# Performance work log

Hardware: AMD Instinct MI355X
Metric: run time of the kernel (lower is better)

## Reference

```python
import jax, jax.numpy as jnp
from jax import lax
import numpy as np

DILATIONS = [2 ** i for i in range(9)] * 2  # 18 layers
WIDTH = 16
K = 3


def softsign(v):
    return v / (1.0 + jnp.abs(v))


def setup_inputs() -> dict:
    key = jax.random.key(0)
    ks = jax.random.split(key, 9)
    B, T = 4, 65536
    n = len(DILATIONS)
    inp = {
        "x": jax.random.normal(ks[0], (B, 1, T), dtype=jnp.float32),
        "start_w": jax.random.normal(ks[1], (WIDTH, 1), dtype=jnp.float32) * 0.5,
        "conv_w": jax.random.normal(ks[2], (n, WIDTH, WIDTH, K), dtype=jnp.float32) * 0.1,
        "conv_b": jax.random.normal(ks[3], (n, WIDTH), dtype=jnp.float32) * 0.1,
        "gate_w": jax.random.normal(ks[4], (n, WIDTH, WIDTH, K), dtype=jnp.float32) * 0.1,
        "gate_b": jax.random.normal(ks[5], (n, WIDTH), dtype=jnp.float32) * 0.1,
        "res_w": jax.random.normal(ks[6], (n - 1, WIDTH, WIDTH), dtype=jnp.float32) * 0.1,
        "res_b": jax.random.normal(ks[7], (n - 1, WIDTH), dtype=jnp.float32) * 0.1,
        "mixer_w": jax.random.normal(ks[8], (1, WIDTH * n), dtype=jnp.float32) * 0.1,
    }
    return inp


def _dilated_causal_conv(h, w, b, d):
    # h: [B,C,T], w: [O,I,K], causal left pad d*(K-1)
    y = lax.conv_general_dilated(
        h, w, window_strides=(1,), padding=[(d * (K - 1), 0)],
        rhs_dilation=(d,), dimension_numbers=("NCH", "OIH", "NCH"))
    return y + b[None, :, None]


def reference(x, start_w, conv_w, conv_b, gate_w, gate_b, res_w, res_b, mixer_w):
    # start 1x1 conv (no bias): [B,1,T] -> [B,W,T]
    h = jnp.einsum("oi,bit->bot", start_w, x)
    outs = []
    n = len(DILATIONS)
    for li, d in enumerate(DILATIONS):
        f = softsign(_dilated_causal_conv(h, conv_w[li], conv_b[li], d))
        g = softsign(_dilated_causal_conv(h, gate_w[li], gate_b[li], d))
        z = f * g
        outs.append(z)
        if li < n - 1:
            h = h + jnp.einsum("oi,bit->bot", res_w[li], z) + res_b[li][None, :, None]
    skip = jnp.concatenate(outs, axis=1)  # [B, W*n, T]
    return jnp.einsum("oc,bct->bot", mixer_w, skip)  # [B,1,T]
```

## Files before the change

kernel.cpp:

```cpp
#include <hip/hip_runtime.h>
#include <hip/hip_bf16.h>
#include <math.h>


typedef __attribute__((ext_vector_type(8))) short short8;
typedef __attribute__((ext_vector_type(4))) unsigned short ushort4v;
typedef __attribute__((ext_vector_type(16))) float f32x16;
typedef unsigned long long u64;

constexpr int TL = 65536;
constexpr int NTOT = 262144;
constexpr int NBLK = 1024;
constexpr size_t PLANE = 4194304;

__device__ __forceinline__ unsigned short f2bf(float v) {
    __hip_bfloat16 b = __float2bfloat16(v);
    unsigned short u; __builtin_memcpy(&u, &b, 2); return u;
}
__device__ __forceinline__ float bf2f(unsigned int u) {
    unsigned int x = (u & 0xffffu) << 16;
    float f; __builtin_memcpy(&f, &x, 4); return f;
}
__device__ __forceinline__ float softsign_f(float v) {
    return v * __builtin_amdgcn_rcpf(1.0f + fabsf(v));
}
__device__ __forceinline__ void spin_on(const unsigned int* f) {
    while (__hip_atomic_load((unsigned int*)f, __ATOMIC_RELAXED,
                             __HIP_MEMORY_SCOPE_AGENT) == 0u) {
        __builtin_amdgcn_s_sleep(8);
    }
}
__device__ __forceinline__ u64 cohload(const unsigned short* p) {
    return __hip_atomic_load((u64*)p, __ATOMIC_RELAXED, __HIP_MEMORY_SCOPE_AGENT);
}
__device__ __forceinline__ void cohstore(unsigned short* p, u64 v) {
    __hip_atomic_store((u64*)p, v, __ATOMIC_RELAXED, __HIP_MEMORY_SCOPE_AGENT);
}

__global__ __launch_bounds__(256) void pack_kernel(
    const float* __restrict__ start_w,
    const float* __restrict__ conv_w,
    const float* __restrict__ gate_w,
    const float* __restrict__ res_w,
    const float* __restrict__ conv_b,
    const float* __restrict__ gate_b,
    unsigned short* __restrict__ bfrag,
    float* __restrict__ fgbias,
    float* __restrict__ rwp,
    float* __restrict__ e0f, float* __restrict__ e0g)
{
    int idx = blockIdx.x * 256 + threadIdx.x;
    if (idx < 55296) {
        int li = idx / 3072, r = idx % 3072;
        int tap = r / 1024, r2 = r % 1024;
        int p = r2 / 512, r3 = r2 % 512;
        int lane = r3 / 8, j = r3 % 8;
        int n = lane & 31, kh = lane >> 5;
        int i_ch = kh * 8 + j, o = n & 15;
        const float* src = (n < 16) ? conv_w : gate_w;
        float w = src[((li * 16 + o) * 16 + i_ch) * 3 + tap];
        unsigned short hi = f2bf(w);
        bfrag[idx] = (p == 0) ? hi : f2bf(w - bf2f(hi));
    } else if (idx < 55296 + 576) {
        int u = idx - 55296; int li = u / 32, n = u % 32;
        fgbias[u] = (n < 16) ? conv_b[li * 16 + n] : gate_b[li * 16 + n - 16];
    } else if (idx < 55296 + 576 + 4352) {
        int u = idx - 55872; int li = u / 256, r = u % 256, i = r / 16, o = r % 16;
        rwp[u] = res_w[(li * 16 + o) * 16 + i];
    } else if (idx < 60320) {
        int u = idx - 60224; int which = u / 48, r = u % 48, k = r / 16, o = r % 16;
        const float* src = which ? gate_w : conv_w;
        float s = 0.f;
        #pragma unroll
        for (int i = 0; i < 16; ++i) s += src[(o * 16 + i) * 3 + k] * start_w[i];
        (which ? e0g : e0f)[k * 16 + o] = s;
    }
}

__global__ __launch_bounds__(256, 4) void wavenet_fused(
    const float* __restrict__ x,
    const float* __restrict__ start_w,
    const float* __restrict__ conv_b,
    const float* __restrict__ gate_b,
    const float* __restrict__ res_b,
    const float* __restrict__ mixer_w,
    const unsigned short* __restrict__ bfrag,
    const float* __restrict__ fgbias,
    const float* __restrict__ rwp,
    const float* __restrict__ e0f,
    const float* __restrict__ e0g,
    unsigned short* __restrict__ pbase,
    float* __restrict__ out,
    unsigned int* __restrict__ flags)
{
    __shared__ float rwl[256];
    __shared__ float sml[64];

    const int td   = threadIdx.x;
    const int wid  = td >> 6;
    const int lane = td & 63;
    const int r0   = lane & 31;
    const int kh   = lane >> 5;
    const int wb   = ((int)blockIdx.x & 7) * (NBLK >> 3) + ((int)blockIdx.x >> 3);
    const int base = wb * 256;

    float skipreg[2];

    {
        unsigned short* h0 = pbase;
        unsigned short* l0 = pbase + PLANE;
        #pragma unroll
        for (int tile = 0; tile < 2; ++tile) {
            const int j = base + tile * 128 + wid * 32 + r0;
            const int t = j & (TL - 1);
            const float x2 = x[j];
            const float x1 = (t >= 1) ? x[j - 1] : 0.f;
            const float x0 = (t >= 2) ? x[j - 2] : 0.f;
            const float xs[3] = {x0, x1, x2};
            float fv[16], qv[16];
            #pragma unroll
            for (int o = 0; o < 16; ++o) { fv[o] = conv_b[o]; qv[o] = gate_b[o]; }
            #pragma unroll
            for (int k = 0; k < 3; ++k) {
                #pragma unroll
                for (int o = 0; o < 16; ++o) {
                    fv[o] += e0f[k * 16 + o] * xs[k];
                    qv[o] += e0g[k * 16 + o] * xs[k];
                }
            }
            float z[16];
            #pragma unroll
            for (int o = 0; o < 16; ++o) z[o] = softsign_f(fv[o]) * softsign_f(qv[o]);
            float s = 0.f;
            #pragma unroll
            for (int o = 0; o < 16; ++o) s += mixer_w[o] * z[o];
            skipreg[tile] = s;
            float hn[16];
            #pragma unroll
            for (int o = 0; o < 16; ++o) hn[o] = start_w[o] * x2 + res_b[o];
            #pragma unroll
            for (int i = 0; i < 16; ++i) {
                #pragma unroll
                for (int o = 0; o < 16; ++o) hn[o] += rwp[i * 16 + o] * z[i];
            }
            if (kh == 0) {
                short8 ph, pl;
                #pragma unroll
                for (int o = 0; o < 8; ++o) {
                    unsigned short u = f2bf(hn[o]);
                    ph[o] = (short)u; pl[o] = (short)f2bf(hn[o] - bf2f(u));
                }
                short8 ph1, pl1;
                #pragma unroll
                for (int o = 0; o < 8; ++o) {
                    unsigned short v = f2bf(hn[8 + o]);
                    ph1[o] = (short)v; pl1[o] = (short)f2bf(hn[8 + o] - bf2f(v));
                }
                u64 w0[2], w1[2], w2[2], w3[2];
                __builtin_memcpy(w0, &ph, 16);
                __builtin_memcpy(w1, &ph1, 16);
                __builtin_memcpy(w2, &pl, 16);
                __builtin_memcpy(w3, &pl1, 16);
                cohstore(h0 + (size_t)j * 16,      w0[0]);
                cohstore(h0 + (size_t)j * 16 + 4,  w0[1]);
                cohstore(h0 + (size_t)j * 16 + 8,  w1[0]);
                cohstore(h0 + (size_t)j * 16 + 12, w1[1]);
                cohstore(l0 + (size_t)j * 16,      w2[0]);
                cohstore(l0 + (size_t)j * 16 + 4,  w2[1]);
                cohstore(l0 + (size_t)j * 16 + 8,  w3[0]);
                cohstore(l0 + (size_t)j * 16 + 12, w3[1]);
            }
        }
    }
    __syncthreads();
    if (td == 0) {
        __hip_atomic_store(&flags[wb], 1u, __ATOMIC_RELAXED, __HIP_MEMORY_SCOPE_AGENT);
    }

    for (int li = 1; li < 18; ++li) {
        const int d = 1 << (li < 9 ? li : li - 9);
        const unsigned short* hin_hi = pbase + (size_t)((li - 1) & 1) * (2 * PLANE);
        const unsigned short* hin_lo = hin_hi + PLANE;
        unsigned short* hout_hi = pbase + (size_t)(li & 1) * (2 * PLANE);
        unsigned short* hout_lo = hout_hi + PLANE;

        if (li < 17) rwl[td] = rwp[li * 256 + td];
        if (td < 16)      sml[td] = mixer_w[li * 16 + td];
        else if (td < 32) sml[td] = (li < 17) ? res_b[li * 16 + td - 16] : 0.f;
        else if (td < 64) sml[td] = fgbias[li * 32 + td - 32];

        if (td == 0 && wb >= 1) spin_on(&flags[(li - 1) * NBLK + wb - 1]);
        if (td == 1 && wb >= 2) spin_on(&flags[(li - 1) * NBLK + wb - 2]);
        if (td == 2 && wb + 1 < NBLK) spin_on(&flags[(li - 1) * NBLK + wb + 1]);
        if (td == 3 && wb + 2 < NBLK) spin_on(&flags[(li - 1) * NBLK + wb + 2]);
        __syncthreads();

        const short8* bfp = (const short8*)(bfrag + li * 3072);
        short8 zero8;
        #pragma unroll
        for (int e = 0; e < 8; ++e) zero8[e] = 0;

        #pragma unroll
        for (int tile = 0; tile < 2; ++tile) {
            const int j = base + tile * 128 + wid * 32 + r0;
            const int t = j & (TL - 1);

            f32x16 acc;
            {
                float4 b0 = *(float4*)&sml[32 + 4 * kh];
                float4 b1 = *(float4*)&sml[40 + 4 * kh];
                float4 b2 = *(float4*)&sml[48 + 4 * kh];
                float4 b3 = *(float4*)&sml[56 + 4 * kh];
                acc[0]=b0.x; acc[1]=b0.y; acc[2]=b0.z; acc[3]=b0.w;
                acc[4]=b1.x; acc[5]=b1.y; acc[6]=b1.z; acc[7]=b1.w;
                acc[8]=b2.x; acc[9]=b2.y; acc[10]=b2.z; acc[11]=b2.w;
                acc[12]=b3.x; acc[13]=b3.y; acc[14]=b3.z; acc[15]=b3.w;
            }

            short8 ah, al;
            #pragma unroll 1
            for (int k = 0; k < 3; ++k) {
                const int off = (k - 2) * d;
                const bool ok = (t + off) >= 0;
                const size_t bofs = (size_t)(ok ? (j + off) : j) * 16 + kh * 8;
                u64 hh[2], ll[2];
                hh[0] = cohload(hin_hi + bofs);
                hh[1] = cohload(hin_hi + bofs + 4);
                ll[0] = cohload(hin_lo + bofs);
                ll[1] = cohload(hin_lo + bofs + 4);
                __builtin_memcpy(&ah, hh, 16);
                __builtin_memcpy(&al, ll, 16);
                if (!ok) { ah = zero8; al = zero8; }
                short8 bh = bfp[(k * 2 + 0) * 64 + lane];
                short8 bl = bfp[(k * 2 + 1) * 64 + lane];
                acc = __builtin_amdgcn_mfma_f32_32x32x16_bf16(bh, ah, acc, 0, 0, 0);
                acc = __builtin_amdgcn_mfma_f32_32x32x16_bf16(bl, ah, acc, 0, 0, 0);
                acc = __builtin_amdgcn_mfma_f32_32x32x16_bf16(bh, al, acc, 0, 0, 0);
            }

            float z8[8];
            #pragma unroll
            for (int r = 0; r < 8; ++r)
                z8[r] = softsign_f(acc[r]) * softsign_f(acc[r + 8]);

            float4 m0 = *(float4*)&sml[4 * kh];
            float4 m1 = *(float4*)&sml[8 + 4 * kh];
            float part = m0.x*z8[0] + m0.y*z8[1] + m0.z*z8[2] + m0.w*z8[3]
                       + m1.x*z8[4] + m1.y*z8[5] + m1.z*z8[6] + m1.w*z8[7];
            float tot = part + __shfl_xor(part, 32);

            if (li == 17) {
                if (kh == 0) out[j] = skipreg[tile] + tot;
            } else {
                if (kh == 0) skipreg[tile] += tot;

                float zo8[8];
                #pragma unroll
                for (int r = 0; r < 8; ++r) zo8[r] = __shfl_xor(z8[r], 32);

                unsigned int uh[4], ul[4];
                __builtin_memcpy(uh, &ah, 16);
                __builtin_memcpy(ul, &al, 16);
                unsigned int sh0 = kh ? uh[0] : uh[2], sh1 = kh ? uh[1] : uh[3];
                unsigned int sl0 = kh ? ul[0] : ul[2], sl1 = kh ? ul[1] : ul[3];
                unsigned int rh0 = (unsigned int)__shfl_xor((int)sh0, 32);
                unsigned int rh1 = (unsigned int)__shfl_xor((int)sh1, 32);
                unsigned int rl0 = (unsigned int)__shfl_xor((int)sl0, 32);
                unsigned int rl1 = (unsigned int)__shfl_xor((int)sl1, 32);
                unsigned int qh0 = kh ? uh[2] : uh[0], qh1 = kh ? uh[3] : uh[1];
                unsigned int ql0 = kh ? ul[2] : ul[0], ql1 = kh ? ul[3] : ul[1];
                unsigned int g1h0 = kh ? rh0 : qh0, g1h1 = kh ? rh1 : qh1;
                unsigned int g2h0 = kh ? qh0 : rh0, g2h1 = kh ? qh1 : rh1;
                unsigned int g1l0 = kh ? rl0 : ql0, g1l1 = kh ? rl1 : ql1;
                unsigned int g2l0 = kh ? ql0 : rl0, g2l1 = kh ? ql1 : rl1;

                float4 rb0 = *(float4*)&sml[16 + 4 * kh];
                float4 rb1 = *(float4*)&sml[24 + 4 * kh];
                float hn[8];
                hn[0] = bf2f(g1h0) + bf2f(g1l0) + rb0.x;
                hn[1] = bf2f(g1h0 >> 16) + bf2f(g1l0 >> 16) + rb0.y;
                hn[2] = bf2f(g1h1) + bf2f(g1l1) + rb0.z;
                hn[3] = bf2f(g1h1 >> 16) + bf2f(g1l1 >> 16) + rb0.w;
                hn[4] = bf2f(g2h0) + bf2f(g2l0) + rb1.x;
                hn[5] = bf2f(g2h0 >> 16) + bf2f(g2l0 >> 16) + rb1.y;
                hn[6] = bf2f(g2h1) + bf2f(g2l1) + rb1.z;
                hn[7] = bf2f(g2h1 >> 16) + bf2f(g2l1 >> 16) + rb1.w;

                #pragma unroll
                for (int i = 0; i < 16; ++i) {
                    const int idx = (i & 3) + 4 * (i >> 3);
                    const int ob  = (i >> 2) & 1;
                    const float zi = (ob == kh) ? z8[idx] : zo8[idx];
                    float4 wA = *(float4*)&rwl[i * 16 + 4 * kh];
                    float4 wB = *(float4*)&rwl[i * 16 + 8 + 4 * kh];
                    hn[0] += wA.x * zi; hn[1] += wA.y * zi;
                    hn[2] += wA.z * zi; hn[3] += wA.w * zi;
                    hn[4] += wB.x * zi; hn[5] += wB.y * zi;
                    hn[6] += wB.z * zi; hn[7] += wB.w * zi;
                }

                ushort4v p1h, p2h, p1l, p2l;
                #pragma unroll
                for (int m = 0; m < 4; ++m) {
                    unsigned short u1 = f2bf(hn[m]);
                    p1h[m] = u1; p1l[m] = f2bf(hn[m] - bf2f(u1));
                    unsigned short u2 = f2bf(hn[4 + m]);
                    p2h[m] = u2; p2l[m] = f2bf(hn[4 + m] - bf2f(u2));
                }
                u64 s0, s1, s2, s3;
                __builtin_memcpy(&s0, &p1h, 8);
                __builtin_memcpy(&s1, &p2h, 8);
                __builtin_memcpy(&s2, &p1l, 8);
                __builtin_memcpy(&s3, &p2l, 8);
                cohstore(hout_hi + (size_t)j * 16 + 4 * kh,     s0);
                cohstore(hout_hi + (size_t)j * 16 + 8 + 4 * kh, s1);
                cohstore(hout_lo + (size_t)j * 16 + 4 * kh,     s2);
                cohstore(hout_lo + (size_t)j * 16 + 8 + 4 * kh, s3);
            }
        }

        if (li < 17) {
            __syncthreads();
            if (td == 0) {
                __hip_atomic_store(&flags[li * NBLK + wb], 1u,
                                   __ATOMIC_RELAXED, __HIP_MEMORY_SCOPE_AGENT);
            }
        }
    }
}

extern "C" void kernel_launch(void* const* d_in, const int* in_sizes, int n_in,
                              void* d_out, int out_size, void* d_ws, size_t ws_size,
                              hipStream_t stream) {
    const float* x       = (const float*)d_in[0];
    const float* start_w = (const float*)d_in[1];
    const float* conv_w  = (const float*)d_in[2];
    const float* conv_b  = (const float*)d_in[3];
    const float* gate_w  = (const float*)d_in[4];
    const float* gate_b  = (const float*)d_in[5];
    const float* res_w   = (const float*)d_in[6];
    const float* res_b   = (const float*)d_in[7];
    const float* mixer_w = (const float*)d_in[8];
    float* out = (float*)d_out;

    float* ws = (float*)d_ws;
    unsigned short* bfrag = (unsigned short*)ws;
    float* fgbias = ws + 27648;
    float* rwp    = fgbias + 576;
    float* e0f    = rwp + 4352;
    float* e0g    = e0f + 48;
    unsigned short* pbase = (unsigned short*)(e0g + 48);
    unsigned int* flags = (unsigned int*)(pbase + 4 * PLANE);
    (void)ws_size; (void)in_sizes; (void)n_in; (void)out_size;

    hipMemsetAsync(flags, 0, 17 * NBLK * sizeof(unsigned int), stream);

    pack_kernel<<<236, 256, 0, stream>>>(start_w, conv_w, gate_w, res_w,
                                         conv_b, gate_b,
                                         bfrag, fgbias, rwp, e0f, e0g);

    wavenet_fused<<<NBLK, 256, 0, stream>>>(
        x, start_w, conv_b, gate_b, res_b, mixer_w,
        bfrag, fgbias, rwp, e0f, e0g, pbase, out, flags);
}
```

Baseline: 370.5 us.

## Route cross-XCD halo rows through coherent buffer, use plain stores elsewhere

```diff
diff --git a/kernel.cpp b/kernel.cpp
--- a/kernel.cpp
+++ b/kernel.cpp
@@ -4,7 +4,6 @@
 
 
 typedef __attribute__((ext_vector_type(8))) short short8;
-typedef __attribute__((ext_vector_type(4))) unsigned short ushort4v;
 typedef __attribute__((ext_vector_type(16))) float f32x16;
 typedef unsigned long long u64;
 
@@ -35,6 +34,16 @@
 }
 __device__ __forceinline__ void cohstore(unsigned short* p, u64 v) {
     __hip_atomic_store((u64*)p, v, __ATOMIC_RELAXED, __HIP_MEMORY_SCOPE_AGENT);
+}
+__device__ __forceinline__ void l2load2(const unsigned short* ph,
+                                        const unsigned short* pl,
+                                        short8& vh, short8& vl) {
+    asm volatile("global_load_dwordx4 %0, %2, off sc0\n\t"
+                 "global_load_dwordx4 %1, %3, off sc0\n\t"
+                 "s_waitcnt vmcnt(0)"
+                 : "=&v"(vh), "=&v"(vl)
+                 : "v"(ph), "v"(pl)
+                 : "memory");
 }
 
 __global__ __launch_bounds__(256) void pack_kernel(
@@ -90,6 +99,7 @@
     const float* __restrict__ e0f,
     const float* __restrict__ e0g,
     unsigned short* __restrict__ pbase,
+    unsigned short* __restrict__ halo,
     float* __restrict__ out,
     unsigned int* __restrict__ flags)
 {
@@ -103,6 +113,7 @@
     const int kh   = lane >> 5;
     const int wb   = ((int)blockIdx.x & 7) * (NBLK >> 3) + ((int)blockIdx.x >> 3);
     const int base = wb * 256;
+    const bool is_halo_prod = (wb & 127) >= 126;
 
     float skipreg[2];
 
@@ -144,31 +155,31 @@
                 for (int o = 0; o < 16; ++o) hn[o] += rwp[i * 16 + o] * z[i];
             }
             if (kh == 0) {
-                short8 ph, pl;
+                u64 wh[4], wl[4];
                 #pragma unroll
-                for (int o = 0; o < 8; ++o) {
-                    unsigned short u = f2bf(hn[o]);
-                    ph[o] = (short)u; pl[o] = (short)f2bf(hn[o] - bf2f(u));
-                }
-                short8 ph1, pl1;
-                #pragma unroll
-                for (int o = 0; o < 8; ++o) {
-                    unsigned short v = f2bf(hn[8 + o]);
-                    ph1[o] = (short)v; pl1[o] = (short)f2bf(hn[8 + o] - bf2f(v));
-                }
-                u64 w0[2], w1[2], w2[2], w3[2];
-                __builtin_memcpy(w0, &ph, 16);
-                __builtin_memcpy(w1, &ph1, 16);
-                __builtin_memcpy(w2, &pl, 16);
-                __builtin_memcpy(w3, &pl1, 16);
-                cohstore(h0 + (size_t)j * 16,      w0[0]);
-                cohstore(h0 + (size_t)j * 16 + 4,  w0[1]);
-                cohstore(h0 + (size_t)j * 16 + 8,  w1[0]);
-                cohstore(h0 + (size_t)j * 16 + 12, w1[1]);
-                cohstore(l0 + (size_t)j * 16,      w2[0]);
-                cohstore(l0 + (size_t)j * 16 + 4,  w2[1]);
-                cohstore(l0 + (size_t)j * 16 + 8,  w3[0]);
-                cohstore(l0 + (size_t)j * 16 + 12, w3[1]);
+                for (int p4 = 0; p4 < 4; ++p4) {
+                    unsigned short hbuf[4], lbuf[4];
+                    #pragma unroll
+                    for (int m = 0; m < 4; ++m) {
+                        unsigned short u = f2bf(hn[p4 * 4 + m]);
+                        hbuf[m] = u; lbuf[m] = f2bf(hn[p4 * 4 + m] - bf2f(u));
+                    }
+                    __builtin_memcpy(&wh[p4], hbuf, 8);
+                    __builtin_memcpy(&wl[p4], lbuf, 8);
+                }
+                u64* dh = (u64*)(h0 + (size_t)j * 16);
+                u64* dl = (u64*)(l0 + (size_t)j * 16);
+                dh[0] = wh[0]; dh[1] = wh[1]; dh[2] = wh[2]; dh[3] = wh[3];
+                dl[0] = wl[0]; dl[1] = wl[1]; dl[2] = wl[2]; dl[3] = wl[3];
+                if (is_halo_prod) {
+                    unsigned short* hb = halo
+                        + (size_t)(wb >> 7) * 16384
+                        + (size_t)((j & 32767) - 32256) * 32;
+                    cohstore(hb + 0,  wh[0]); cohstore(hb + 4,  wh[1]);
+                    cohstore(hb + 8,  wh[2]); cohstore(hb + 12, wh[3]);
+                    cohstore(hb + 16, wl[0]); cohstore(hb + 20, wl[1]);
+                    cohstore(hb + 24, wl[2]); cohstore(hb + 28, wl[3]);
+                }
             }
         }
     }
@@ -183,6 +194,8 @@
         const unsigned short* hin_lo = hin_hi + PLANE;
         unsigned short* hout_hi = pbase + (size_t)(li & 1) * (2 * PLANE);
         unsigned short* hout_lo = hout_hi + PLANE;
+        const unsigned short* halo_in = halo + (size_t)((li - 1) & 1) * 131072;
+        unsigned short* halo_out = halo + (size_t)(li & 1) * 131072;
 
         if (li < 17) rwl[td] = rwp[li * 256 + td];
         if (td < 16)      sml[td] = mixer_w[li * 16 + td];
@@ -222,15 +235,25 @@
             for (int k = 0; k < 3; ++k) {
                 const int off = (k - 2) * d;
                 const bool ok = (t + off) >= 0;
-                const size_t bofs = (size_t)(ok ? (j + off) : j) * 16 + kh * 8;
-                u64 hh[2], ll[2];
-                hh[0] = cohload(hin_hi + bofs);
-                hh[1] = cohload(hin_hi + bofs + 4);
-                ll[0] = cohload(hin_lo + bofs);
-                ll[1] = cohload(hin_lo + bofs + 4);
-                __builtin_memcpy(&ah, hh, 16);
-                __builtin_memcpy(&al, ll, 16);
-                if (!ok) { ah = zero8; al = zero8; }
+                const int rrow = ok ? (j + off) : j;
+                short8 ah_, al_;
+                if (ok && ((rrow >> 15) != (j >> 15))) {
+                    const unsigned short* hb = halo_in
+                        + (size_t)(rrow >> 15) * 16384
+                        + (size_t)((rrow & 32767) - 32256) * 32;
+                    u64 hh[2], ll[2];
+                    hh[0] = cohload(hb + 8 * kh);
+                    hh[1] = cohload(hb + 8 * kh + 4);
+                    ll[0] = cohload(hb + 16 + 8 * kh);
+                    ll[1] = cohload(hb + 16 + 8 * kh + 4);
+                    __builtin_memcpy(&ah_, hh, 16);
+                    __builtin_memcpy(&al_, ll, 16);
+                } else {
+                    const size_t bofs = (size_t)rrow * 16 + kh * 8;
+                    l2load2(hin_hi + bofs, hin_lo + bofs, ah_, al_);
+                    if (!ok) { ah_ = zero8; al_ = zero8; }
+                }
+                ah = ah_; al = al_;
                 short8 bh = bfp[(k * 2 + 0) * 64 + lane];
                 short8 bl = bfp[(k * 2 + 1) * 64 + lane];
                 acc = __builtin_amdgcn_mfma_f32_32x32x16_bf16(bh, ah, acc, 0, 0, 0);
@@ -299,23 +322,34 @@
                     hn[6] += wB.z * zi; hn[7] += wB.w * zi;
                 }
 
-                ushort4v p1h, p2h, p1l, p2l;
-                #pragma unroll
-                for (int m = 0; m < 4; ++m) {
-                    unsigned short u1 = f2bf(hn[m]);
-                    p1h[m] = u1; p1l[m] = f2bf(hn[m] - bf2f(u1));
-                    unsigned short u2 = f2bf(hn[4 + m]);
-                    p2h[m] = u2; p2l[m] = f2bf(hn[4 + m] - bf2f(u2));
-                }
                 u64 s0, s1, s2, s3;
-                __builtin_memcpy(&s0, &p1h, 8);
-                __builtin_memcpy(&s1, &p2h, 8);
-                __builtin_memcpy(&s2, &p1l, 8);
-                __builtin_memcpy(&s3, &p2l, 8);
-                cohstore(hout_hi + (size_t)j * 16 + 4 * kh,     s0);
-                cohstore(hout_hi + (size_t)j * 16 + 8 + 4 * kh, s1);
-                cohstore(hout_lo + (size_t)j * 16 + 4 * kh,     s2);
-                cohstore(hout_lo + (size_t)j * 16 + 8 + 4 * kh, s3);
+                {
+                    unsigned short b0[4], b1[4], b2[4], b3[4];
+                    #pragma unroll
+                    for (int m = 0; m < 4; ++m) {
+                        unsigned short u1 = f2bf(hn[m]);
+                        b0[m] = u1; b2[m] = f2bf(hn[m] - bf2f(u1));
+                        unsigned short u2 = f2bf(hn[4 + m]);
+                        b1[m] = u2; b3[m] = f2bf(hn[4 + m] - bf2f(u2));
+                    }
+                    __builtin_memcpy(&s0, b0, 8);
+                    __builtin_memcpy(&s1, b1, 8);
+                    __builtin_memcpy(&s2, b2, 8);
+                    __builtin_memcpy(&s3, b3, 8);
+                }
+                *(u64*)(hout_hi + (size_t)j * 16 + 4 * kh)     = s0;
+                *(u64*)(hout_hi + (size_t)j * 16 + 8 + 4 * kh) = s1;
+                *(u64*)(hout_lo + (size_t)j * 16 + 4 * kh)     = s2;
+                *(u64*)(hout_lo + (size_t)j * 16 + 8 + 4 * kh) = s3;
+                if (is_halo_prod) {
+                    unsigned short* hb = halo_out
+                        + (size_t)(wb >> 7) * 16384
+                        + (size_t)((j & 32767) - 32256) * 32;
+                    cohstore(hb + 4 * kh,          s0);
+                    cohstore(hb + 8 + 4 * kh,      s1);
+                    cohstore(hb + 16 + 4 * kh,     s2);
+                    cohstore(hb + 16 + 8 + 4 * kh, s3);
+                }
             }
         }
 
@@ -350,7 +384,8 @@
     float* e0f    = rwp + 4352;
     float* e0g    = e0f + 48;
     unsigned short* pbase = (unsigned short*)(e0g + 48);
-    unsigned int* flags = (unsigned int*)(pbase + 4 * PLANE);
+    unsigned short* halo  = pbase + 4 * PLANE;
+    unsigned int* flags = (unsigned int*)(halo + 262144);
     (void)ws_size; (void)in_sizes; (void)n_in; (void)out_size;
 
     hipMemsetAsync(flags, 0, 17 * NBLK * sizeof(unsigned int), stream);
@@ -361,5 +396,5 @@
 
     wavenet_fused<<<NBLK, 256, 0, stream>>>(
         x, start_w, conv_b, gate_b, res_b, mixer_w,
-        bfrag, fgbias, rwp, e0f, e0g, pbase, out, flags);
-}
+        bfrag, fgbias, rwp, e0f, e0g, pbase, halo, out, flags);
+}
```

After: 308.6 us. 16.7% less time.
